# Performance work log

Measured on AMD Instinct MI355X. Metric: run time of the kernel, lower is better.

## Reference

```python
import jax, jax.numpy as jnp
import numpy as np

B, S, D = 4, 2048, 1024


def setup_inputs() -> dict:
    key = jax.random.key(0)
    ks = jax.random.split(key, 11)
    sc = 0.02
    f32 = jnp.float32
    return {
        "x1": jax.random.normal(ks[0], (B, S, D), f32),
        "x2": jax.random.normal(ks[1], (B, S, D), f32),
        "x3": jax.random.normal(ks[2], (B, S, D), f32),
        # Stacked per-modality projection weights, stored (in, out) so y = x @ W + b
        "Wq": jax.random.normal(ks[3], (3, D, D), f32) * sc,
        "bq": jax.random.normal(ks[4], (3, D), f32) * sc,
        "Wk": jax.random.normal(ks[5], (3, D, D), f32) * sc,
        "bk": jax.random.normal(ks[6], (3, D), f32) * sc,
        "Wv": jax.random.normal(ks[7], (3, D, D), f32) * sc,
        "bv": jax.random.normal(ks[8], (3, D), f32) * sc,
        "Wo": jax.random.normal(ks[9], (3, 2 * D, D), f32) * sc,
        "bo": jax.random.normal(ks[10], (3, D), f32) * sc,
    }


def reference(x1, x2, x3, Wq, bq, Wk, bk, Wv, bv, Wo, bo):
    x = jnp.stack([x1, x2, x3])                      # (3, B, S, D)
    q = jnp.einsum('mbsd,mde->mbse', x, Wq) + bq[:, None, None, :]
    k = jnp.einsum('mbsd,mde->mbse', x, Wk) + bk[:, None, None, :]
    v = jnp.einsum('mbsd,mde->mbse', x, Wv) + bv[:, None, None, :]
    scale = 1.0 / jnp.sqrt(jnp.asarray(x.shape[-1], x.dtype))
    # self-scores per modality: q_i @ k_i^T
    scores = jnp.einsum('mbsd,mbtd->mbst', q, k) * scale   # (3, B, S, S)
    attn = jax.nn.softmax(scores, axis=-1)
    # context_i = attn_i @ v_{(i+1) mod 3}  (1->2, 2->3, 3->1); dropout is eval-mode identity
    v_next = jnp.roll(v, shift=-1, axis=0)
    ctx = jnp.einsum('mbst,mbtd->mbsd', attn, v_next)      # (3, B, S, D)
    comb = jnp.concatenate([x, ctx], axis=-1)              # (3, B, S, 2D)
    out = jnp.einsum('mbsf,mfd->mbsd', comb, Wo) + bo[:, None, None, :]
    global_feature = jnp.concatenate([out[0], out[1], out[2]], axis=1)  # (B, 3S, D)
    return out[0], out[1], out[2], global_feature
```

## Files before the change

### kernel.cpp

```cpp
#include <hip/hip_runtime.h>
#include <hip/hip_bf16.h>

typedef __bf16 bf16_t;
typedef __bf16 bf16x8 __attribute__((ext_vector_type(8)));
typedef float f32x4 __attribute__((ext_vector_type(4)));

typedef __attribute__((address_space(1))) unsigned int as1_uint;
typedef __attribute__((address_space(3))) unsigned int as3_uint;

#define Bsz 4
#define Ssz 2048
#define Dsz 1024
#define BSD (Bsz * Ssz * Dsz)
#define SCALE_ 0.03125f

__device__ __forceinline__ void gll16(const void* g, void* l) {
  __builtin_amdgcn_global_load_lds((const as1_uint*)g, (as3_uint*)l, 16, 0, 0);
}

__device__ __forceinline__ unsigned bfbits(float f) {
  union { bf16_t h; unsigned short u; } c;
  c.h = (bf16_t)f;
  return (unsigned)c.u;
}

__device__ __forceinline__ void xcd_swz(int bx, int by, int GX, int GY,
                                        int* nx, int* ny) {
  const int L = bx + GX * by;
  const int xcd = L & 7, idx = L >> 3;
  *nx = idx % GX;
  *ny = (GY >> 3) * xcd + idx / GX;
}

__device__ __forceinline__ void gemm_core(char* AsB, char* BsB,
                                          const bf16_t* A, const bf16_t* A2, int ksplit,
                                          int lda, int lda2,
                                          const bf16_t* Bt, int ldb,
                                          int ktiles, f32x4 acc[4][4]) {
  const int tid = threadIdx.x;
  const int wave = tid >> 6, lane = tid & 63;
  const int quad = lane >> 4, m16 = lane & 15, x7 = lane & 7;
  const int waveM = (wave >> 1) << 6, waveN = (wave & 1) << 6;
  const int srow = tid >> 3;
  const int schunk = (tid & 7) ^ ((tid >> 3) & 7);
  const int ldsbase = wave << 10;

  for (int kt = 0; kt < ktiles; ++kt) {
    const bf16_t* Ak = (kt < ksplit) ? (A + kt * 64) : (A2 + (kt - ksplit) * 64);
    const int ldak = (kt < ksplit) ? lda : lda2;
    const bf16_t* Bk = Bt + kt * 64;
    __syncthreads();
#pragma unroll
    for (int it = 0; it < 4; ++it)
      gll16(Ak + (size_t)(it * 32 + srow) * ldak + schunk * 8, AsB + it * 4096 + ldsbase);
#pragma unroll
    for (int it = 0; it < 4; ++it)
      gll16(Bk + (size_t)(it * 32 + srow) * ldb + schunk * 8, BsB + it * 4096 + ldsbase);
    __syncthreads();
#pragma unroll
    for (int t = 0; t < 2; ++t) {
      bf16x8 a[4], b[4];
      const int cc = t * 4 + quad;
#pragma unroll
      for (int i = 0; i < 4; ++i) {
        const int rr = waveM + i * 16 + m16;
        a[i] = *(const bf16x8*)(AsB + rr * 128 + ((cc ^ x7) << 4));
      }
#pragma unroll
      for (int j = 0; j < 4; ++j) {
        const int rr = waveN + j * 16 + m16;
        b[j] = *(const bf16x8*)(BsB + rr * 128 + ((cc ^ x7) << 4));
      }
#pragma unroll
      for (int i = 0; i < 4; ++i)
#pragma unroll
        for (int j = 0; j < 4; ++j)
          acc[i][j] = __builtin_amdgcn_mfma_f32_16x16x32_bf16(b[j], a[i], acc[i][j], 0, 0, 0);
    }
  }
}

__device__ __forceinline__ ushort4 pack4(const f32x4 v, const float4 b) {
  ushort4 u;
  u.x = (unsigned short)bfbits(v[0] + b.x);
  u.y = (unsigned short)bfbits(v[1] + b.y);
  u.z = (unsigned short)bfbits(v[2] + b.z);
  u.w = (unsigned short)bfbits(v[3] + b.w);
  return u;
}

__global__ __launch_bounds__(256, 4)
void gemm_bt_bf16(const bf16_t* __restrict__ A, long long sAz, int lda,
                  const bf16_t* __restrict__ Bt, long long sBz, int ldb,
                  bf16_t* __restrict__ C, long long sCz, int ldc,
                  int K, int rollB, float* sums, int mode) {
  __shared__ __attribute__((aligned(16))) char smem[32768];
  const int z = blockIdx.z;
  int zb = z;
  if (rollB) { const int m = z >> 2, b = z & 3; zb = ((m + 1) % 3) * Bsz + b; }
  int nx, ny;
  xcd_swz(blockIdx.x, blockIdx.y, gridDim.x, gridDim.y, &nx, &ny);
  const bf16_t* Az = A + (long long)z * sAz + (size_t)ny * 128 * lda;
  const bf16_t* Bz = Bt + (long long)zb * sBz + (size_t)nx * 128 * ldb;
  f32x4 acc[4][4];
  const f32x4 zero = {0.f, 0.f, 0.f, 0.f};
#pragma unroll
  for (int i = 0; i < 4; ++i)
#pragma unroll
    for (int j = 0; j < 4; ++j) acc[i][j] = zero;

  gemm_core(smem, smem + 16384, Az, Az, 1 << 30, lda, lda, Bz, ldb, K / 64, acc);

  const int lane = threadIdx.x & 63, wave = threadIdx.x >> 6;
  const int Mb = ny * 128 + ((wave >> 1) << 6) + (lane & 15);
  const int Nb = nx * 128 + ((wave & 1) << 6) + ((lane >> 4) << 2);
  bf16_t* Cz = C + (long long)z * sCz;

  if (mode == 1) {
    float* sz = sums + (size_t)z * Ssz;
#pragma unroll
    for (int i = 0; i < 4; ++i) {
      const int M = Mb + i * 16;
      float rs = 0.f;
#pragma unroll
      for (int j = 0; j < 4; ++j) {
        const int N = Nb + j * 16;
        float e0 = __expf(acc[i][j][0] * SCALE_);
        float e1 = __expf(acc[i][j][1] * SCALE_);
        float e2 = __expf(acc[i][j][2] * SCALE_);
        float e3 = __expf(acc[i][j][3] * SCALE_);
        rs += e0 + e1 + e2 + e3;
        ushort4 u;
        u.x = (unsigned short)bfbits(e0); u.y = (unsigned short)bfbits(e1);
        u.z = (unsigned short)bfbits(e2); u.w = (unsigned short)bfbits(e3);
        *(ushort4*)(Cz + (size_t)M * ldc + N) = u;
      }
      rs += __shfl_xor(rs, 16);
      rs += __shfl_xor(rs, 32);
      if (lane < 16) atomicAdd(sz + M, rs);
    }
  } else if (mode == 2) {
    const float* sz = sums + (size_t)z * Ssz;
#pragma unroll
    for (int i = 0; i < 4; ++i) {
      const int M = Mb + i * 16;
      const float inv = 1.0f / sz[M];
#pragma unroll
      for (int j = 0; j < 4; ++j) {
        const int N = Nb + j * 16;
        ushort4 u;
        u.x = (unsigned short)bfbits(acc[i][j][0] * inv);
        u.y = (unsigned short)bfbits(acc[i][j][1] * inv);
        u.z = (unsigned short)bfbits(acc[i][j][2] * inv);
        u.w = (unsigned short)bfbits(acc[i][j][3] * inv);
        *(ushort4*)(Cz + (size_t)M * ldc + N) = u;
      }
    }
  } else {
    const float4 zb4 = {0.f, 0.f, 0.f, 0.f};
#pragma unroll
    for (int i = 0; i < 4; ++i) {
      const int M = Mb + i * 16;
#pragma unroll
      for (int j = 0; j < 4; ++j) {
        const int N = Nb + j * 16;
        *(ushort4*)(Cz + (size_t)M * ldc + N) = pack4(acc[i][j], zb4);
      }
    }
  }
}

__global__ __launch_bounds__(256, 4)
void gemm_qkv(const bf16_t* __restrict__ xb, const bf16_t* __restrict__ Wqkvt,
              const float* __restrict__ bq, const float* __restrict__ bk,
              const float* __restrict__ bvp,
              bf16_t* __restrict__ Q, bf16_t* __restrict__ Kb, bf16_t* __restrict__ Vt) {
  __shared__ __attribute__((aligned(16))) char smem[34048];
  const int m = blockIdx.z;
  const int x = blockIdx.x;
  const int which = x >> 3;
  const bf16_t* Az = xb + (size_t)m * BSD + (size_t)blockIdx.y * 128 * Dsz;
  const bf16_t* Bz = Wqkvt + (size_t)m * 3145728 + (size_t)x * 131072;
  f32x4 acc[4][4];
  const f32x4 zero = {0.f, 0.f, 0.f, 0.f};
#pragma unroll
  for (int i = 0; i < 4; ++i)
#pragma unroll
    for (int j = 0; j < 4; ++j) acc[i][j] = zero;

  gemm_core(smem, smem + 16384, Az, Az, 1 << 30, Dsz, Dsz, Bz, Dsz, 16, acc);

  const int tid = threadIdx.x;
  const int lane = tid & 63, wave = tid >> 6;
  const int Ml = ((wave >> 1) << 6) + (lane & 15);
  const int Nl = ((wave & 1) << 6) + ((lane >> 4) << 2);
  const int dseg0 = (x & 7) * 128;
  const float* bb = (which == 0 ? bq : which == 1 ? bk : bvp) + m * Dsz;

  if (which < 2) {
    bf16_t* Cz = (which == 0 ? Q : Kb) + (size_t)m * BSD;
#pragma unroll
    for (int j = 0; j < 4; ++j) {
      const int N = Nl + j * 16;
      const float4 b4 = *(const float4*)(bb + dseg0 + N);
#pragma unroll
      for (int i = 0; i < 4; ++i) {
        const int M = blockIdx.y * 128 + Ml + i * 16;
        *(ushort4*)(Cz + (size_t)M * Dsz + dseg0 + N) = pack4(acc[i][j], b4);
      }
    }
  } else {
    unsigned short* T = (unsigned short*)smem;
    __syncthreads();
#pragma unroll
    for (int j = 0; j < 4; ++j) {
      const int N = Nl + j * 16;
      const float4 b4 = *(const float4*)(bb + dseg0 + N);
      const float bia[4] = {b4.x, b4.y, b4.z, b4.w};
#pragma unroll
      for (int i = 0; i < 4; ++i) {
        const int M = Ml + i * 16;
#pragma unroll
        for (int r = 0; r < 4; ++r)
          T[(N + r) * 132 + M] = (unsigned short)bfbits(acc[i][j][r] + bia[r]);
      }
    }
    __syncthreads();
    const int b = blockIdx.y >> 4;
    const int s0 = (blockIdx.y & 15) * 128;
    bf16_t* Vz = Vt + ((size_t)(m * 4 + b) * 1024 + dseg0) * Ssz;
#pragma unroll
    for (int e = 0; e < 16; ++e) {
      const int idx = e * 256 + tid;
      const int nl = idx >> 5, mc = (idx & 31) * 4;
      const ushort4 u = *(const ushort4*)(T + nl * 132 + mc);
      *(ushort4*)(Vz + (size_t)nl * Ssz + s0 + mc) = u;
    }
  }
}

__global__ __launch_bounds__(256, 4)
void gemm_out(const bf16_t* __restrict__ xb, const bf16_t* __restrict__ ctx,
              const bf16_t* __restrict__ Wot, const float* __restrict__ bo,
              float* __restrict__ out) {
  __shared__ __attribute__((aligned(16))) char smem[32768];
  const int m = blockIdx.z;
  int nx, ny;
  xcd_swz(blockIdx.x, blockIdx.y, 8, 64, &nx, &ny);
  const bf16_t* Az = xb + (size_t)m * BSD + (size_t)ny * 128 * Dsz;
  const bf16_t* A2z = ctx + (size_t)m * BSD + (size_t)ny * 128 * Dsz;
  const bf16_t* Bz = Wot + (size_t)m * (Dsz * 2 * Dsz) + (size_t)nx * 128 * (2 * Dsz);
  f32x4 acc[4][4];
  const f32x4 zero = {0.f, 0.f, 0.f, 0.f};
#pragma unroll
  for (int i = 0; i < 4; ++i)
#pragma unroll
    for (int j = 0; j < 4; ++j) acc[i][j] = zero;

  gemm_core(smem, smem + 16384, Az, A2z, 16, Dsz, Dsz, Bz, 2 * Dsz, 32, acc);

  const int lane = threadIdx.x & 63, wave = threadIdx.x >> 6;
  const int Mb = ny * 128 + ((wave >> 1) << 6) + (lane & 15);
  const int Nb = nx * 128 + ((wave & 1) << 6) + ((lane >> 4) << 2);
  const float* bz = bo + m * Dsz;
#pragma unroll
  for (int i = 0; i < 4; ++i) {
    const int M = Mb + i * 16;
    const int b = M >> 11, s = M & 2047;
    float* o1 = out + (size_t)m * BSD + (size_t)M * Dsz;
    float* o2 = out + (size_t)3 * BSD + (size_t)b * (3 * Ssz * Dsz) + (size_t)(m * Ssz + s) * Dsz;
#pragma unroll
    for (int j = 0; j < 4; ++j) {
      const int N = Nb + j * 16;
      const float4 b4 = *(const float4*)(bz + N);
      float4 o;
      o.x = acc[i][j][0] + b4.x; o.y = acc[i][j][1] + b4.y;
      o.z = acc[i][j][2] + b4.z; o.w = acc[i][j][3] + b4.w;
      *(float4*)(o1 + N) = o;
      *(float4*)(o2 + N) = o;
    }
  }
}

__global__ __launch_bounds__(256)
void cvt_x(const float* __restrict__ x1, const float* __restrict__ x2,
           const float* __restrict__ x3, bf16_t* __restrict__ xb) {
  const size_t i = ((size_t)blockIdx.x * 256 + threadIdx.x) * 4;
  const float* src;
  size_t off;
  if (i < (size_t)BSD)          { src = x1; off = i; }
  else if (i < (size_t)2 * BSD) { src = x2; off = i - BSD; }
  else                          { src = x3; off = i - (size_t)2 * BSD; }
  const float4 v = *(const float4*)(src + off);
  union { bf16_t h[4]; uint2 u; } o;
  o.h[0] = (bf16_t)v.x; o.h[1] = (bf16_t)v.y; o.h[2] = (bf16_t)v.z; o.h[3] = (bf16_t)v.w;
  *(uint2*)(xb + i) = o.u;
}

__global__ __launch_bounds__(256)
void transpose_to_bf16(const float* __restrict__ in, bf16_t* __restrict__ out,
                       int ldin, int ldout, long long sIn, long long sOut) {
  __shared__ bf16_t Ts[64][65];
  const int t = threadIdx.x;
  const long long z = blockIdx.z;
  const float* inz = in + z * sIn;
  bf16_t* outz = out + z * sOut;
  const int r0 = blockIdx.y << 6, c0 = blockIdx.x << 6;
#pragma unroll
  for (int e = 0; e < 4; ++e) {
    const int idx = (e * 256 + t) * 4;
    const int rr = idx >> 6, cc = idx & 63;
    const float4 v = *(const float4*)(inz + (size_t)(r0 + rr) * ldin + (c0 + cc));
    Ts[rr][cc] = (bf16_t)v.x; Ts[rr][cc + 1] = (bf16_t)v.y;
    Ts[rr][cc + 2] = (bf16_t)v.z; Ts[rr][cc + 3] = (bf16_t)v.w;
  }
  __syncthreads();
#pragma unroll
  for (int e = 0; e < 4; ++e) {
    const int idx = (e * 256 + t) * 4;
    const int oc = idx >> 6, orr = idx & 63;
    union { bf16_t h[4]; uint2 u; } o4;
    o4.h[0] = Ts[orr][oc]; o4.h[1] = Ts[orr + 1][oc];
    o4.h[2] = Ts[orr + 2][oc]; o4.h[3] = Ts[orr + 3][oc];
    *(uint2*)(outz + (size_t)(c0 + oc) * ldout + (r0 + orr)) = o4.u;
  }
}

__global__ __launch_bounds__(256)
void zero_f32(float* __restrict__ p, int n) {
  const int i = blockIdx.x * 256 + threadIdx.x;
  if (i < n) p[i] = 0.f;
}

extern "C" void kernel_launch(void* const* d_in, const int* in_sizes, int n_in,
                              void* d_out, int out_size, void* d_ws, size_t ws_size,
                              hipStream_t stream) {
  const float* x1 = (const float*)d_in[0];
  const float* x2 = (const float*)d_in[1];
  const float* x3 = (const float*)d_in[2];
  const float* Wq = (const float*)d_in[3];
  const float* bq = (const float*)d_in[4];
  const float* Wk = (const float*)d_in[5];
  const float* bk = (const float*)d_in[6];
  const float* Wv = (const float*)d_in[7];
  const float* bv = (const float*)d_in[8];
  const float* Wo = (const float*)d_in[9];
  const float* bo = (const float*)d_in[10];

  char* ws = (char*)d_ws;
  bf16_t* xb    = (bf16_t*)(ws + 0);
  bf16_t* Wqkvt = (bf16_t*)(ws + 50331648);
  bf16_t* Wot   = (bf16_t*)(ws + 69206016);
  bf16_t* Q     = (bf16_t*)(ws + 81788928);
  bf16_t* Kb    = (bf16_t*)(ws + 132120576);
  bf16_t* Vt    = (bf16_t*)(ws + 182452224);
  bf16_t* Sc    = (bf16_t*)d_out;
  bf16_t* ctx   = Q;
  float* sums = (float*)d_out + (size_t)3 * BSD;

  cvt_x<<<24576, 256, 0, stream>>>(x1, x2, x3, xb);
  zero_f32<<<96, 256, 0, stream>>>(sums, 12 * Ssz);
  transpose_to_bf16<<<dim3(16, 16, 3), 256, 0, stream>>>(Wq, Wqkvt + 0,       1024, 1024, 1048576LL, 3145728LL);
  transpose_to_bf16<<<dim3(16, 16, 3), 256, 0, stream>>>(Wk, Wqkvt + 1048576, 1024, 1024, 1048576LL, 3145728LL);
  transpose_to_bf16<<<dim3(16, 16, 3), 256, 0, stream>>>(Wv, Wqkvt + 2097152, 1024, 1024, 1048576LL, 3145728LL);
  transpose_to_bf16<<<dim3(16, 32, 3), 256, 0, stream>>>(Wo, Wot, 1024, 2048, 2097152LL, 2097152LL);
  gemm_qkv<<<dim3(24, 64, 3), 256, 0, stream>>>(xb, Wqkvt, bq, bk, bv, Q, Kb, Vt);
  gemm_bt_bf16<<<dim3(16, 16, 12), 256, 0, stream>>>(Q, 2097152LL, Dsz, Kb, 2097152LL, Dsz, Sc, 4194304LL, Ssz, Dsz, 0, sums, 1);
  gemm_bt_bf16<<<dim3(8, 16, 12), 256, 0, stream>>>(Sc, 4194304LL, Ssz, Vt, 2097152LL, Ssz, ctx, 2097152LL, Dsz, Ssz, 1, sums, 2);
  gemm_out<<<dim3(8, 64, 3), 256, 0, stream>>>(xb, ctx, Wot, bo, (float*)d_out);
}
```

Measured before the change: 838.8 us.

## Fold Wq·Wkᵀ into a single matrix to drop the K projection

Computes M = Wq·Wkᵀ per modality, so scores become (x·M)·xᵀ instead of projecting Q and K separately. The K GEMM is removed and Q is computed against the combined matrix. The row-softmax-invariant bias terms are dropped, and the row-varying term x·(Wk·bq) is added back through a per-column vector c inside the exp epilogue. This adds a small D×D GEMM per modality and changes bf16 rounding, since M is formed from bf16 weights and rounded to bf16 before use. There is also no max-subtraction, so the larger logits carry overflow risk.

```diff
diff --git a/kernel.cpp b/kernel.cpp
--- a/kernel.cpp
+++ b/kernel.cpp
@@ -93,7 +93,7 @@
 void gemm_bt_bf16(const bf16_t* __restrict__ A, long long sAz, int lda,
                   const bf16_t* __restrict__ Bt, long long sBz, int ldb,
                   bf16_t* __restrict__ C, long long sCz, int ldc,
-                  int K, int rollB, float* sums, int mode) {
+                  int K, int rollB, float* sums, const float* cvec, int mode) {
   __shared__ __attribute__((aligned(16))) char smem[32768];
   const int z = blockIdx.z;
   int zb = z;
@@ -118,6 +118,10 @@
 
   if (mode == 1) {
     float* sz = sums + (size_t)z * Ssz;
+    const float* cz = cvec + (size_t)z * Ssz;
+    float4 c4[4];
+#pragma unroll
+    for (int j = 0; j < 4; ++j) c4[j] = *(const float4*)(cz + Nb + j * 16);
 #pragma unroll
     for (int i = 0; i < 4; ++i) {
       const int M = Mb + i * 16;
@@ -125,10 +129,10 @@
 #pragma unroll
       for (int j = 0; j < 4; ++j) {
         const int N = Nb + j * 16;
-        float e0 = __expf(acc[i][j][0] * SCALE_);
-        float e1 = __expf(acc[i][j][1] * SCALE_);
-        float e2 = __expf(acc[i][j][2] * SCALE_);
-        float e3 = __expf(acc[i][j][3] * SCALE_);
+        float e0 = __expf((acc[i][j][0] + c4[j].x) * SCALE_);
+        float e1 = __expf((acc[i][j][1] + c4[j].y) * SCALE_);
+        float e2 = __expf((acc[i][j][2] + c4[j].z) * SCALE_);
+        float e3 = __expf((acc[i][j][3] + c4[j].w) * SCALE_);
         rs += e0 + e1 + e2 + e3;
         ushort4 u;
         u.x = (unsigned short)bfbits(e0); u.y = (unsigned short)bfbits(e1);
@@ -171,16 +175,15 @@
 }
 
 __global__ __launch_bounds__(256, 4)
-void gemm_qkv(const bf16_t* __restrict__ xb, const bf16_t* __restrict__ Wqkvt,
-              const float* __restrict__ bq, const float* __restrict__ bk,
-              const float* __restrict__ bvp,
-              bf16_t* __restrict__ Q, bf16_t* __restrict__ Kb, bf16_t* __restrict__ Vt) {
+void gemm_qv(const bf16_t* __restrict__ xb, const bf16_t* __restrict__ mw,
+             const float* __restrict__ bvp,
+             bf16_t* __restrict__ Q, bf16_t* __restrict__ Vt) {
   __shared__ __attribute__((aligned(16))) char smem[34048];
   const int m = blockIdx.z;
   const int x = blockIdx.x;
   const int which = x >> 3;
   const bf16_t* Az = xb + (size_t)m * BSD + (size_t)blockIdx.y * 128 * Dsz;
-  const bf16_t* Bz = Wqkvt + (size_t)m * 3145728 + (size_t)x * 131072;
+  const bf16_t* Bz = mw + (size_t)m * 2097152 + (size_t)x * 131072;
   f32x4 acc[4][4];
   const f32x4 zero = {0.f, 0.f, 0.f, 0.f};
 #pragma unroll
@@ -195,21 +198,21 @@
   const int Ml = ((wave >> 1) << 6) + (lane & 15);
   const int Nl = ((wave & 1) << 6) + ((lane >> 4) << 2);
   const int dseg0 = (x & 7) * 128;
-  const float* bb = (which == 0 ? bq : which == 1 ? bk : bvp) + m * Dsz;
-
-  if (which < 2) {
-    bf16_t* Cz = (which == 0 ? Q : Kb) + (size_t)m * BSD;
+
+  if (which == 0) {
+    bf16_t* Cz = Q + (size_t)m * BSD;
+    const float4 z4 = {0.f, 0.f, 0.f, 0.f};
 #pragma unroll
     for (int j = 0; j < 4; ++j) {
       const int N = Nl + j * 16;
-      const float4 b4 = *(const float4*)(bb + dseg0 + N);
 #pragma unroll
       for (int i = 0; i < 4; ++i) {
         const int M = blockIdx.y * 128 + Ml + i * 16;
-        *(ushort4*)(Cz + (size_t)M * Dsz + dseg0 + N) = pack4(acc[i][j], b4);
+        *(ushort4*)(Cz + (size_t)M * Dsz + dseg0 + N) = pack4(acc[i][j], z4);
       }
     }
   } else {
+    const float* bb = bvp + m * Dsz;
     unsigned short* T = (unsigned short*)smem;
     __syncthreads();
 #pragma unroll
@@ -283,18 +286,60 @@
 }
 
 __global__ __launch_bounds__(256)
-void cvt_x(const float* __restrict__ x1, const float* __restrict__ x2,
-           const float* __restrict__ x3, bf16_t* __restrict__ xb) {
+void ucomp(const float* __restrict__ Wk, const float* __restrict__ bq,
+           float* __restrict__ u) {
+  const int wave = threadIdx.x >> 6, lane = threadIdx.x & 63;
+  const int row = blockIdx.x * 4 + wave;
+  const int m = row >> 10, d = row & 1023;
+  const float* wr = Wk + (size_t)m * 1048576 + (size_t)d * 1024;
+  const float* bz = bq + m * 1024;
+  float s = 0.f;
+#pragma unroll
+  for (int k = 0; k < 4; ++k) {
+    const float4 w = *(const float4*)(wr + (lane + k * 64) * 4);
+    const float4 bb = *(const float4*)(bz + (lane + k * 64) * 4);
+    s += w.x * bb.x + w.y * bb.y + w.z * bb.z + w.w * bb.w;
+  }
+  for (int o = 32; o > 0; o >>= 1) s += __shfl_xor(s, o);
+  if (lane == 0) u[row] = s;
+}
+
+__global__ __launch_bounds__(256)
+void cvt_x_c(const float* __restrict__ x1, const float* __restrict__ x2,
+             const float* __restrict__ x3, bf16_t* __restrict__ xb,
+             const float* __restrict__ u, float* __restrict__ c) {
+  const int row = blockIdx.x;
+  const int m = row >> 13;
+  const int r = row & 8191;
+  const int tid = threadIdx.x;
+  const float* src = (m == 0 ? x1 : m == 1 ? x2 : x3) + (size_t)r * 1024 + tid * 4;
+  const float4 v = *(const float4*)src;
+  union { bf16_t h[4]; uint2 uu; } o;
+  o.h[0] = (bf16_t)v.x; o.h[1] = (bf16_t)v.y; o.h[2] = (bf16_t)v.z; o.h[3] = (bf16_t)v.w;
+  *(uint2*)(xb + (size_t)row * 1024 + tid * 4) = o.uu;
+  const float4 uv = *(const float4*)(u + m * 1024 + tid * 4);
+  float s = v.x * uv.x + v.y * uv.y + v.z * uv.z + v.w * uv.w;
+  for (int o2 = 32; o2 > 0; o2 >>= 1) s += __shfl_xor(s, o2);
+  __shared__ float red[4];
+  if ((tid & 63) == 0) red[tid >> 6] = s;
+  __syncthreads();
+  if (tid == 0) {
+    const int b = r >> 11, ss = r & 2047;
+    c[(size_t)(m * 4 + b) * Ssz + ss] = red[0] + red[1] + red[2] + red[3];
+  }
+}
+
+__global__ __launch_bounds__(256)
+void cvt_w2(const float* __restrict__ Wq, const float* __restrict__ Wk,
+            bf16_t* __restrict__ Wqb, bf16_t* __restrict__ Wkb) {
   const size_t i = ((size_t)blockIdx.x * 256 + threadIdx.x) * 4;
-  const float* src;
-  size_t off;
-  if (i < (size_t)BSD)          { src = x1; off = i; }
-  else if (i < (size_t)2 * BSD) { src = x2; off = i - BSD; }
-  else                          { src = x3; off = i - (size_t)2 * BSD; }
+  const float* src; bf16_t* dst; size_t off;
+  if (i < (size_t)3145728) { src = Wq; dst = Wqb; off = i; }
+  else                     { src = Wk; dst = Wkb; off = i - 3145728; }
   const float4 v = *(const float4*)(src + off);
   union { bf16_t h[4]; uint2 u; } o;
   o.h[0] = (bf16_t)v.x; o.h[1] = (bf16_t)v.y; o.h[2] = (bf16_t)v.z; o.h[3] = (bf16_t)v.w;
-  *(uint2*)(xb + i) = o.u;
+  *(uint2*)(dst + off) = o.u;
 }
 
 __global__ __launch_bounds__(256)
@@ -346,26 +391,31 @@
   const float* bv = (const float*)d_in[8];
   const float* Wo = (const float*)d_in[9];
   const float* bo = (const float*)d_in[10];
+  (void)bk;
 
   char* ws = (char*)d_ws;
   bf16_t* xb    = (bf16_t*)(ws + 0);
-  bf16_t* Wqkvt = (bf16_t*)(ws + 50331648);
-  bf16_t* Wot   = (bf16_t*)(ws + 69206016);
-  bf16_t* Q     = (bf16_t*)(ws + 81788928);
-  bf16_t* Kb    = (bf16_t*)(ws + 132120576);
-  bf16_t* Vt    = (bf16_t*)(ws + 182452224);
+  bf16_t* MtWv  = (bf16_t*)(ws + 50331648);
+  bf16_t* Wot   = (bf16_t*)(ws + 62914560);
+  bf16_t* Q     = (bf16_t*)(ws + 75497472);
+  bf16_t* Vt    = (bf16_t*)(ws + 125829120);
+  bf16_t* Wqb   = (bf16_t*)(ws + 176160768);
+  bf16_t* Wkb   = (bf16_t*)(ws + 182452224);
+  float*  u     = (float*)(ws + 188743680);
+  float*  c     = (float*)(ws + 188755968);
   bf16_t* Sc    = (bf16_t*)d_out;
   bf16_t* ctx   = Q;
   float* sums = (float*)d_out + (size_t)3 * BSD;
 
-  cvt_x<<<24576, 256, 0, stream>>>(x1, x2, x3, xb);
+  ucomp<<<768, 256, 0, stream>>>(Wk, bq, u);
+  cvt_x_c<<<24576, 256, 0, stream>>>(x1, x2, x3, xb, u, c);
   zero_f32<<<96, 256, 0, stream>>>(sums, 12 * Ssz);
-  transpose_to_bf16<<<dim3(16, 16, 3), 256, 0, stream>>>(Wq, Wqkvt + 0,       1024, 1024, 1048576LL, 3145728LL);
-  transpose_to_bf16<<<dim3(16, 16, 3), 256, 0, stream>>>(Wk, Wqkvt + 1048576, 1024, 1024, 1048576LL, 3145728LL);
-  transpose_to_bf16<<<dim3(16, 16, 3), 256, 0, stream>>>(Wv, Wqkvt + 2097152, 1024, 1024, 1048576LL, 3145728LL);
+  cvt_w2<<<6144, 256, 0, stream>>>(Wq, Wk, Wqb, Wkb);
+  transpose_to_bf16<<<dim3(16, 16, 3), 256, 0, stream>>>(Wv, MtWv + 1048576, 1024, 1024, 1048576LL, 2097152LL);
   transpose_to_bf16<<<dim3(16, 32, 3), 256, 0, stream>>>(Wo, Wot, 1024, 2048, 2097152LL, 2097152LL);
-  gemm_qkv<<<dim3(24, 64, 3), 256, 0, stream>>>(xb, Wqkvt, bq, bk, bv, Q, Kb, Vt);
-  gemm_bt_bf16<<<dim3(16, 16, 12), 256, 0, stream>>>(Q, 2097152LL, Dsz, Kb, 2097152LL, Dsz, Sc, 4194304LL, Ssz, Dsz, 0, sums, 1);
-  gemm_bt_bf16<<<dim3(8, 16, 12), 256, 0, stream>>>(Sc, 4194304LL, Ssz, Vt, 2097152LL, Ssz, ctx, 2097152LL, Dsz, Ssz, 1, sums, 2);
+  gemm_bt_bf16<<<dim3(8, 8, 3), 256, 0, stream>>>(Wkb, 1048576LL, Dsz, Wqb, 1048576LL, Dsz, MtWv, 2097152LL, Dsz, Dsz, 0, sums, c, 0);
+  gemm_qv<<<dim3(16, 64, 3), 256, 0, stream>>>(xb, MtWv, bv, Q, Vt);
+  gemm_bt_bf16<<<dim3(16, 16, 12), 256, 0, stream>>>(Q, 2097152LL, Dsz, xb, 2097152LL, Dsz, Sc, 4194304LL, Ssz, Dsz, 0, sums, c, 1);
+  gemm_bt_bf16<<<dim3(8, 16, 12), 256, 0, stream>>>(Sc, 4194304LL, Ssz, Vt, 2097152LL, Ssz, ctx, 2097152LL, Dsz, Ssz, 1, sums, c, 2);
   gemm_out<<<dim3(8, 64, 3), 256, 0, stream>>>(xb, ctx, Wot, bo, (float*)d_out);
 }
```

Measured after the change: 809.2 us. 1.04x faster.
